# Performance work log

Measured on AMD Instinct MI355X. Metric: run time of the kernel, lower is better.

The kernel has to match this reference:

```python
import jax, jax.numpy as jnp
import numpy as np

N = 100000
E = 1600000
H = 128
IN = 16
OUT = 16
L = 3
G = 256  # number of graphs
EPS = 1e-12


def setup_inputs() -> dict:
    key = jax.random.key(0)
    ks = jax.random.split(key, 24)
    s = 0.05
    inp = {
        "x": jax.random.normal(ks[0], (N, IN), jnp.float32),
        "pos": jax.random.normal(ks[1], (N, 3), jnp.float32),
        "edge_index": jax.random.randint(ks[2], (2, E), 0, N, jnp.int64),
        "batch": jnp.sort(jax.random.randint(ks[3], (N,), 0, G, jnp.int64)),
        # node_lin: Linear(IN,H), ReLU, Linear(H,H)
        "node_W1": jax.random.normal(ks[4], (IN, H), jnp.float32) * s,
        "node_b1": jnp.zeros((H,), jnp.float32),
        "node_W2": jax.random.normal(ks[5], (H, H), jnp.float32) * s,
        "node_b2": jnp.zeros((H,), jnp.float32),
        # per-layer local_nn: Linear(H+4,H), ReLU, Linear(H,H)  (stacked over L)
        "local_W1": jax.random.normal(ks[6], (L, H + 4, H), jnp.float32) * s,
        "local_b1": jnp.zeros((L, H), jnp.float32),
        "local_W2": jax.random.normal(ks[7], (L, H, H), jnp.float32) * s,
        "local_b2": jnp.zeros((L, H), jnp.float32),
        # per-layer global_nn: Linear(H,H), ReLU, Linear(H,H)
        "global_W1": jax.random.normal(ks[8], (L, H, H), jnp.float32) * s,
        "global_b1": jnp.zeros((L, H), jnp.float32),
        "global_W2": jax.random.normal(ks[9], (L, H, H), jnp.float32) * s,
        "global_b2": jnp.zeros((L, H), jnp.float32),
        # heads
        "lin1_W": jax.random.normal(ks[10], (H, H // 2), jnp.float32) * s,
        "lin1_b": jnp.zeros((H // 2,), jnp.float32),
        "lin2_W": jax.random.normal(ks[11], (H // 2, OUT), jnp.float32) * s,
        "lin2_b": jnp.zeros((OUT,), jnp.float32),
    }
    return inp


def _angle(v1, v2):
    c = jnp.cross(v1, v2, axis=1)
    return jnp.arctan2(jnp.linalg.norm(c, axis=1), jnp.sum(v1 * v2, axis=1))


def reference(x, pos, edge_index, batch,
              node_W1, node_b1, node_W2, node_b2,
              local_W1, local_b1, local_W2, local_b2,
              global_W1, global_b1, global_W2, global_b2,
              lin1_W, lin1_b, lin2_W, lin2_b):
    src = edge_index[0]  # j (source)
    dst = edge_index[1]  # i (target, aggregation index)

    normal = pos / (jnp.linalg.norm(pos, axis=-1, keepdims=True) + EPS)

    pos_i, pos_j = pos[dst], pos[src]
    n_i, n_j = normal[dst], normal[src]
    pseudo = pos_j - pos_i  # [E, 3]
    # point-pair features [E, 4] (constant across layers since pos is fixed)
    ppf = jnp.stack([
        jnp.linalg.norm(pseudo, axis=1),
        _angle(n_i, pseudo),
        _angle(n_j, pseudo),
        _angle(n_i, n_j),
    ], axis=1)

    # node_lin (x is 2D -> MLP path; embedding path unused)
    h = jax.nn.relu(x @ node_W1 + node_b1) @ node_W2 + node_b2  # [N, H]

    for l in range(L):
        msg = jnp.concatenate([h[src], ppf], axis=1)  # [E, H+4]
        msg = jax.nn.relu(msg @ local_W1[l] + local_b1[l]) @ local_W2[l] + local_b2[l]
        agg = jax.ops.segment_sum(msg, dst, num_segments=N)  # scatter-add to nodes
        h = jax.nn.relu(agg @ global_W1[l] + global_b1[l]) @ global_W2[l] + global_b2[l]
        h = jax.nn.relu(h)

    out = jax.nn.relu(h @ lin1_W + lin1_b) @ lin2_W + lin2_b  # [N, OUT]
    return jax.ops.segment_sum(out, batch, num_segments=G)  # [G, OUT]
```

## Files before the change

kernel.cpp:

```cpp
#include <hip/hip_runtime.h>

#define NN 100000
#define NE 1600000
#define HD 128
#define NL 3
#define NG 256
#define NB 196
#define BCAP 56
#define BCAPTOT 10240

typedef __attribute__((ext_vector_type(8))) short short8;
typedef __attribute__((ext_vector_type(4))) float floatx4;
typedef __attribute__((ext_vector_type(2))) _Float16 half2v;

static __device__ __forceinline__ unsigned short f2bf(float f) {
    unsigned int u = __float_as_uint(f);
    u += 0x7fffu + ((u >> 16) & 1u);
    return (unsigned short)(u >> 16);
}
static __device__ __forceinline__ float bf2f(unsigned short h) {
    return __uint_as_float(((unsigned int)h) << 16);
}
static __device__ __forceinline__ float angle3(float ax, float ay, float az,
                                               float bx, float by, float bz) {
    float cx = ay*bz - az*by;
    float cy = az*bx - ax*bz;
    float cz = ax*by - ay*bx;
    float cn = sqrtf(cx*cx + cy*cy + cz*cz);
    float d  = ax*bx + ay*by + az*bz;
    return atan2f(cn, d);
}

union U32H2 { unsigned int u; half2v h; };
static __device__ __forceinline__ half2v u2h(unsigned int x) { U32H2 t; t.u = x; return t.h; }
static __device__ __forceinline__ unsigned int h2u(half2v x) { U32H2 t; t.h = x; return t.u; }


struct PrepSrcs { const float* p[14]; };

__global__ void k_prep(PrepSrcs s, unsigned short* __restrict__ dst) {
    int mat = blockIdx.y;
    int N = (mat == 13) ? 64 : 128;
    int e = blockIdx.x * 256 + threadIdx.x;
    if (e >= N * 128) return;
    int n = e >> 7, k = e & 127;
    dst[mat * 16384 + n * 128 + k] = f2bf(s.p[mat][k * N + n]);
}


__global__ void k_pn(const float* __restrict__ pos, float4* __restrict__ pn, int n) {
    int i = blockIdx.x * blockDim.x + threadIdx.x;
    if (i >= n) return;
    float x = pos[3*i], y = pos[3*i+1], z = pos[3*i+2];
    float inv = 1.0f / (sqrtf(x*x + y*y + z*z) + 1e-12f);
    pn[2*i]   = make_float4(x, y, z, 0.0f);
    pn[2*i+1] = make_float4(x*inv, y*inv, z*inv, 0.0f);
}


__global__ void k_binit(int* __restrict__ bcursor) {
    int b = threadIdx.x;
    if (b < NB) bcursor[b] = b * BCAPTOT;
}

__global__ __launch_bounds__(256) void k_bscatter(const int* __restrict__ ei,
                                                  int* __restrict__ bcursor,
                                                  unsigned int* __restrict__ bids, int e) {
    __shared__ int lcnt[NB];
    __shared__ unsigned int lbuf[NB * BCAP];
    int tid = threadIdx.x;
    for (int i = tid; i < NB; i += 256) lcnt[i] = 0;
    __syncthreads();
    int i0 = blockIdx.x * 4096 + tid * 16;
    if (i0 < e) {
#pragma unroll
        for (int q = 0; q < 4; q++) {
            int4 s4 = *(const int4*)(ei + i0 + q * 4);
            int4 d4 = *(const int4*)(ei + NE + i0 + q * 4);
            int ds[4] = {d4.x, d4.y, d4.z, d4.w};
            int ss[4] = {s4.x, s4.y, s4.z, s4.w};
#pragma unroll
            for (int r = 0; r < 4; r++) {
                int d = ds[r];
                int b = d >> 9;
                unsigned int w = ((unsigned int)(d & 511) << 17) | (unsigned int)ss[r];
                int pos = atomicAdd(&lcnt[b], 1);
                if (pos < BCAP) lbuf[b * BCAP + pos] = w;
                else { int p = atomicAdd(&bcursor[b], 1); bids[p] = w; }
            }
        }
    }
    __syncthreads();
    if (tid < NB) {
        int c = lcnt[tid];
        if (c > BCAP) c = BCAP;
        if (c > 0) {
            int base = atomicAdd(&bcursor[tid], c);
            for (int k = 0; k < c; k++) bids[base + k] = lbuf[tid * BCAP + k];
        }
    }
}

__global__ __launch_bounds__(256) void k_bfinal(const unsigned int* __restrict__ bids,
                                                const int* __restrict__ bcursor,
                                                int* __restrict__ ssrc,
                                                int* __restrict__ sdst,
                                                int* __restrict__ starts,
                                                int* __restrict__ deg) {
    __shared__ int s1[512];
    __shared__ int s2[256];
    int tid = threadIdx.x;
    int b = blockIdx.x;
    int node0 = b << 9;
    int base0 = b * BCAPTOT;
    int cnt = bcursor[b] - base0;
    s1[2 * tid] = 0; s1[2 * tid + 1] = 0;
    __syncthreads();
    for (int j = tid; j < cnt; j += 256)
        atomicAdd(&s1[bids[base0 + j] >> 17], 1);
    __syncthreads();
    int a0 = s1[2 * tid], a1 = s1[2 * tid + 1];
    s2[tid] = a0 + a1;
    __syncthreads();
    for (int off = 1; off < 256; off <<= 1) {
        int v = (tid >= off) ? s2[tid - off] : 0;
        __syncthreads();
        s2[tid] += v;
        __syncthreads();
    }
    int pairBase = (tid ? s2[tid - 1] : 0);
    int e0 = base0 + pairBase;
    int e1 = e0 + a0;
    int n0 = node0 + 2 * tid;
    if (n0 < NN)     { starts[n0] = e0;     deg[n0] = a0; }
    if (n0 + 1 < NN) { starts[n0 + 1] = e1; deg[n0 + 1] = a1; }
    s1[2 * tid] = e0; s1[2 * tid + 1] = e1;
    __syncthreads();
    for (int j = tid; j < cnt; j += 256) {
        unsigned int w = bids[base0 + j];
        int loc = w >> 17;
        int src = (int)(w & 0x1ffffu);
        int p = atomicAdd(&s1[loc], 1);
        ssrc[p] = src;
        sdst[p] = node0 + loc;
    }
}

__global__ void k_ppf_sorted(const int* __restrict__ ssrc, const int* __restrict__ sdst,
                             const float4* __restrict__ pn,
                             uint2* __restrict__ sppf, int npos) {
    int j = blockIdx.x * blockDim.x + threadIdx.x;
    if (j >= npos) return;
    unsigned int s = (unsigned int)ssrc[j];
    unsigned int d = (unsigned int)sdst[j];
    if (s >= NN || d >= NN) return;
    float4 ps_ = pn[2*s], ns_ = pn[2*s+1];
    float4 pd_ = pn[2*d], nd_ = pn[2*d+1];
    float px = ps_.x - pd_.x;
    float py = ps_.y - pd_.y;
    float pz = ps_.z - pd_.z;
    float f0 = sqrtf(px*px + py*py + pz*pz);
    float f1 = angle3(nd_.x, nd_.y, nd_.z, px, py, pz);
    float f2 = angle3(ns_.x, ns_.y, ns_.z, px, py, pz);
    float f3 = angle3(nd_.x, nd_.y, nd_.z, ns_.x, ns_.y, ns_.z);
    half2v h01 = { (_Float16)f0, (_Float16)f1 };
    half2v h23 = { (_Float16)f2, (_Float16)f3 };
    uint2 w;
    w.x = h2u(h01);
    w.y = h2u(h23);
    sppf[j] = w;
}


__global__ void k_node_lin1(const float* __restrict__ x, const float* __restrict__ W1,
                            const float* __restrict__ b1, unsigned short* __restrict__ u, int n) {
    __shared__ float sW[16 * HD];
    __shared__ float sb[HD];
    __shared__ float sx[16 * 16];
    int tid = threadIdx.x;
    for (int idx = tid; idx < 16 * HD; idx += 256) sW[idx] = W1[idx];
    if (tid < HD) sb[tid] = b1[tid];
    int r0 = blockIdx.x * 16;
    for (int idx = tid; idx < 16 * 16; idx += 256) {
        int r = r0 + (idx >> 4);
        sx[idx] = (r < n) ? x[r * 16 + (idx & 15)] : 0.0f;
    }
    __syncthreads();
    int col = tid & 127;
    int rsub = tid >> 7;
    float wcol[16];
#pragma unroll
    for (int k = 0; k < 16; k++) wcol[k] = sW[k * HD + col];
    float bb = sb[col];
    for (int rr = rsub; rr < 16; rr += 2) {
        int r = r0 + rr;
        if (r >= n) break;
        float acc = bb;
#pragma unroll
        for (int k = 0; k < 16; k++) acc = fmaf(sx[rr * 16 + k], wcol[k], acc);
        u[r * HD + col] = f2bf(fmaxf(acc, 0.0f));
    }
}


#define SKT 136

struct ChainArgs {
    const unsigned short* W[4];
    const float* bias[4];
    int epi[4];
};

template <int NS, int NCL>
__global__ __launch_bounds__(256, 4) void k_chain(
    const unsigned short* __restrict__ in, ChainArgs ca,
    const int* __restrict__ deg, unsigned short* __restrict__ out, int n) {
    __shared__ unsigned short LB[128 * SKT];
    __shared__ float sbias[NS][128];
    int tid = threadIdx.x;
    int wave = tid >> 6, lane = tid & 63, quad = lane >> 4, m = lane & 15;
    int rowBase = wave * 32;
    int gBase = blockIdx.x * 128;
    floatx4 z = {0.0f, 0.0f, 0.0f, 0.0f};
    short8 a[2][4];
#pragma unroll
    for (int rt = 0; rt < 2; rt++) {
        int r = gBase + rowBase + rt * 16 + m;
        int rc = r < n ? r : n - 1;
        const unsigned short* ap = in + (size_t)rc * 128 + quad * 8;
#pragma unroll
        for (int s = 0; s < 4; s++) a[rt][s] = *(const short8*)(ap + s * 32);
    }
    if (tid < 128) {
#pragma unroll
        for (int s = 0; s < NS; s++)
            if (ca.epi[s]) sbias[s][tid] = ca.bias[s][tid];
    }
    float dvd[2][4];
#pragma unroll
    for (int rt = 0; rt < 2; rt++)
#pragma unroll
        for (int r = 0; r < 4; r++) {
            int gr = gBase + rowBase + rt * 16 + quad * 4 + r;
            dvd[rt][r] = (float)deg[gr < n ? gr : n - 1];
        }

#pragma unroll
    for (int st = 0; st < NS; st++) {
        const int NC = (st == NS - 1) ? NCL : 128;
        if (st > 0) {
#pragma unroll
            for (int rt = 0; rt < 2; rt++) {
                const unsigned short* tp = &LB[(rowBase + rt * 16 + m) * SKT + quad * 8];
#pragma unroll
                for (int s = 0; s < 4; s++) a[rt][s] = *(const short8*)(tp + s * 32);
            }
            __syncthreads();
        }
        for (int idx = tid; idx < NC * 16; idx += 256) {
            int c = idx >> 4, k8 = idx & 15;
            *(short8*)&LB[c * SKT + k8 * 8] = ((const short8*)ca.W[st])[idx];
        }
        __syncthreads();

        floatx4 acc[2][8];
#pragma unroll
        for (int rt = 0; rt < 2; rt++)
#pragma unroll
            for (int ct = 0; ct < 8; ct++) acc[rt][ct] = z;
#pragma unroll
        for (int ct = 0; ct < NC / 16; ct++) {
            const unsigned short* bp = &LB[(ct * 16 + m) * SKT + quad * 8];
#pragma unroll
            for (int s = 0; s < 4; s++) {
                short8 b = *(const short8*)(bp + s * 32);
                acc[0][ct] = __builtin_amdgcn_mfma_f32_16x16x32_bf16(a[0][s], b, acc[0][ct], 0, 0, 0);
                acc[1][ct] = __builtin_amdgcn_mfma_f32_16x16x32_bf16(a[1][s], b, acc[1][ct], 0, 0, 0);
            }
        }
        __syncthreads();

        int epi = ca.epi[st];
#pragma unroll
        for (int ct = 0; ct < NC / 16; ct++) {
            int col = ct * 16 + m;
            float bv = epi ? sbias[st][col] : 0.0f;
#pragma unroll
            for (int rt = 0; rt < 2; rt++) {
#pragma unroll
                for (int r = 0; r < 4; r++) {
                    float v = acc[rt][ct][r];
                    if (epi == 1) v += bv;
                    else if (epi == 2) v += dvd[rt][r] * bv;
                    else if (epi == 3) v = fmaxf(v + bv, 0.0f);
                    unsigned short bw = f2bf(v);
                    int row = rowBase + rt * 16 + quad * 4 + r;
                    if (st == NS - 1) {
                        int gr = gBase + row;
                        if (gr < n) out[(size_t)gr * NCL + col] = bw;
                    } else {
                        LB[row * SKT + col] = bw;
                    }
                }
            }
        }
        if (st < NS - 1) __syncthreads();
    }
}


#if __has_builtin(__builtin_amdgcn_fdot2)
#define HAVE_FDOT2 1
#else
#define HAVE_FDOT2 0
#endif

static __device__ __forceinline__ void agg_edge(unsigned int u, uint2 q,
                                                half2v wA0, half2v wB0, half2v wA1, half2v wB1,
                                                float& a0, float& a1) {
    float tlo = __uint_as_float(u << 16);
    float thi = __uint_as_float(u & 0xffff0000u);
#if HAVE_FDOT2
    half2v p01 = u2h(q.x), p23 = u2h(q.y);
    float g0 = __builtin_amdgcn_fdot2(p01, wA0,
               __builtin_amdgcn_fdot2(p23, wB0, tlo, false), false);
    float g1 = __builtin_amdgcn_fdot2(p01, wA1,
               __builtin_amdgcn_fdot2(p23, wB1, thi, false), false);
#else
    half2v p01 = u2h(q.x), p23 = u2h(q.y);
    float px = (float)p01.x, py = (float)p01.y, pz = (float)p23.x, pw = (float)p23.y;
    float g0 = fmaf(px, (float)wA0.x, fmaf(py, (float)wA0.y,
               fmaf(pz, (float)wB0.x, fmaf(pw, (float)wB0.y, tlo))));
    float g1 = fmaf(px, (float)wA1.x, fmaf(py, (float)wA1.y,
               fmaf(pz, (float)wB1.x, fmaf(pw, (float)wB1.y, thi))));
#endif
    a0 += fmaxf(g0, 0.0f);
    a1 += fmaxf(g1, 0.0f);
}

#define GLOAD(u, off) \
    __asm__ volatile("global_load_dword %0, %1, %2" : "=v"(u) : "v"(off), "s"(t))

__global__ __launch_bounds__(256, 8) void k_agg(
    const int* __restrict__ starts, const int* __restrict__ deg,
    const int* __restrict__ ssrc,
    const uint2* __restrict__ sppf, const unsigned int* __restrict__ t,
    const float* __restrict__ W1p,
    unsigned int* __restrict__ S, int n) {
    int node = (blockIdx.x * 256 + threadIdx.x) >> 6;
    if (node >= n) return;
    int lane = threadIdx.x & 63;
    int c2 = lane * 2;
    float2 w0 = *(const float2*)(W1p + c2);
    float2 w1 = *(const float2*)(W1p + 128 + c2);
    float2 w2 = *(const float2*)(W1p + 256 + c2);
    float2 w3 = *(const float2*)(W1p + 384 + c2);
    half2v wA0 = { (_Float16)w0.x, (_Float16)w1.x };
    half2v wB0 = { (_Float16)w2.x, (_Float16)w3.x };
    half2v wA1 = { (_Float16)w0.y, (_Float16)w1.y };
    half2v wB1 = { (_Float16)w2.y, (_Float16)w3.y };
    int e0 = __builtin_amdgcn_readfirstlane(starts[node]);
    int dg = __builtin_amdgcn_readfirstlane(deg[node]);
    int e1 = e0 + dg;
    unsigned int lane4 = (unsigned int)lane * 4u;
    float a0 = 0.0f, a1 = 0.0f;
    int e = e0;
    for (; e + 8 <= e1; e += 8) {
        int s0 = ssrc[e],     s1 = ssrc[e + 1], s2 = ssrc[e + 2], s3 = ssrc[e + 3];
        int s4 = ssrc[e + 4], s5 = ssrc[e + 5], s6 = ssrc[e + 6], s7 = ssrc[e + 7];
        uint2 q0 = sppf[e],     q1 = sppf[e + 1], q2 = sppf[e + 2], q3 = sppf[e + 3];
        uint2 q4 = sppf[e + 4], q5 = sppf[e + 5], q6 = sppf[e + 6], q7 = sppf[e + 7];
        unsigned int u0, u1, u2, u3, u4, u5, u6, u7;
        GLOAD(u0, ((unsigned)s0 << 8) | lane4);
        GLOAD(u1, ((unsigned)s1 << 8) | lane4);
        GLOAD(u2, ((unsigned)s2 << 8) | lane4);
        GLOAD(u3, ((unsigned)s3 << 8) | lane4);
        GLOAD(u4, ((unsigned)s4 << 8) | lane4);
        GLOAD(u5, ((unsigned)s5 << 8) | lane4);
        GLOAD(u6, ((unsigned)s6 << 8) | lane4);
        GLOAD(u7, ((unsigned)s7 << 8) | lane4);
        __asm__ volatile("s_waitcnt vmcnt(0)"
                         : "+v"(u0), "+v"(u1), "+v"(u2), "+v"(u3),
                           "+v"(u4), "+v"(u5), "+v"(u6), "+v"(u7));
        agg_edge(u0, q0, wA0, wB0, wA1, wB1, a0, a1);
        agg_edge(u1, q1, wA0, wB0, wA1, wB1, a0, a1);
        agg_edge(u2, q2, wA0, wB0, wA1, wB1, a0, a1);
        agg_edge(u3, q3, wA0, wB0, wA1, wB1, a0, a1);
        agg_edge(u4, q4, wA0, wB0, wA1, wB1, a0, a1);
        agg_edge(u5, q5, wA0, wB0, wA1, wB1, a0, a1);
        agg_edge(u6, q6, wA0, wB0, wA1, wB1, a0, a1);
        agg_edge(u7, q7, wA0, wB0, wA1, wB1, a0, a1);
    }
    if (e + 4 <= e1) {
        int s0 = ssrc[e], s1 = ssrc[e + 1], s2 = ssrc[e + 2], s3 = ssrc[e + 3];
        uint2 q0 = sppf[e], q1 = sppf[e + 1], q2 = sppf[e + 2], q3 = sppf[e + 3];
        unsigned int u0, u1, u2, u3;
        GLOAD(u0, ((unsigned)s0 << 8) | lane4);
        GLOAD(u1, ((unsigned)s1 << 8) | lane4);
        GLOAD(u2, ((unsigned)s2 << 8) | lane4);
        GLOAD(u3, ((unsigned)s3 << 8) | lane4);
        __asm__ volatile("s_waitcnt vmcnt(0)"
                         : "+v"(u0), "+v"(u1), "+v"(u2), "+v"(u3));
        agg_edge(u0, q0, wA0, wB0, wA1, wB1, a0, a1);
        agg_edge(u1, q1, wA0, wB0, wA1, wB1, a0, a1);
        agg_edge(u2, q2, wA0, wB0, wA1, wB1, a0, a1);
        agg_edge(u3, q3, wA0, wB0, wA1, wB1, a0, a1);
        e += 4;
    }
    for (; e < e1; e++) {
        int s0 = ssrc[e];
        uint2 q0 = sppf[e];
        unsigned int u0 = t[((unsigned)s0 << 6) | lane];
        agg_edge(u0, q0, wA0, wB0, wA1, wB1, a0, a1);
    }
    unsigned int r = ((unsigned int)f2bf(a1) << 16) | f2bf(a0);
    S[(size_t)node * 64 + lane] = r;
}


__global__ void k_head2(const unsigned short* __restrict__ v, const float* __restrict__ W,
                        const float* __restrict__ b, const int* __restrict__ batch,
                        float* __restrict__ outg, int n) {
    __shared__ float sW[64 * 16];
    __shared__ float sb[16];
    __shared__ float sacc[64][17];
    __shared__ int sbid[64];
    int tid = threadIdx.x;
    for (int idx = tid; idx < 64 * 16; idx += 256) sW[idx] = W[idx];
    if (tid < 16) sb[tid] = b[tid];
    int r0 = blockIdx.x * 64;
    if (tid < 64) {
        int r = r0 + tid;
        sbid[tid] = (r < n) ? batch[r] : -1;
    }
    __syncthreads();
    int rl = tid >> 4, c = tid & 15;
#pragma unroll
    for (int i = 0; i < 4; i++) {
        int row = rl + i * 16;
        int r = r0 + row;
        float acc = 0.0f;
        if (r < n) {
            const unsigned int* vr = (const unsigned int*)(v + (size_t)r * 64);
            acc = sb[c];
#pragma unroll
            for (int k2 = 0; k2 < 32; k2++) {
                unsigned int u = vr[k2];
                acc = fmaf(__uint_as_float(u << 16), sW[(2 * k2) * 16 + c], acc);
                acc = fmaf(__uint_as_float(u & 0xffff0000u), sW[(2 * k2 + 1) * 16 + c], acc);
            }
        }
        sacc[row][c] = acc;
    }
    __syncthreads();
    if (tid < 16) {
        int cc = tid;
        float run = 0.0f;
        int cur = sbid[0];
        for (int row = 0; row < 64; row++) {
            int bid = sbid[row];
            if (bid != cur) {
                if (cur >= 0) atomicAdd(&outg[cur * 16 + cc], run);
                run = 0.0f;
                cur = bid;
            }
            run += sacc[row][cc];
        }
        if (cur >= 0) atomicAdd(&outg[cur * 16 + cc], run);
    }
}


extern "C" void kernel_launch(void* const* d_in, const int* in_sizes, int n_in,
                              void* d_out, int out_size, void* d_ws, size_t ws_size,
                              hipStream_t stream) {
    (void)in_sizes; (void)n_in; (void)out_size; (void)ws_size;
    const float* x    = (const float*)d_in[0];
    const float* pos  = (const float*)d_in[1];
    const int*   ei   = (const int*)d_in[2];
    const int*   batch= (const int*)d_in[3];
    const float* nW1  = (const float*)d_in[4];
    const float* nb1  = (const float*)d_in[5];
    const float* nW2  = (const float*)d_in[6];
    const float* nb2  = (const float*)d_in[7];
    const float* lW1  = (const float*)d_in[8];
    const float* lb1  = (const float*)d_in[9];
    const float* lW2  = (const float*)d_in[10];
    const float* lb2  = (const float*)d_in[11];
    const float* gW1  = (const float*)d_in[12];
    const float* gb1  = (const float*)d_in[13];
    const float* gW2  = (const float*)d_in[14];
    const float* gb2  = (const float*)d_in[15];
    const float* l1W  = (const float*)d_in[16];
    const float* l1b  = (const float*)d_in[17];
    const float* l2W  = (const float*)d_in[18];
    const float* l2b  = (const float*)d_in[19];
    float* outg = (float*)d_out;

    const int NPOS = NB * BCAPTOT;

    char* ws = (char*)d_ws;
    size_t off = 0;
    auto alloc = [&](size_t bytes) -> void* {
        void* p = ws + off;
        off = (off + bytes + 255) & ~(size_t)255;
        return p;
    };
    unsigned short* P0 = (unsigned short*)alloc((size_t)NN * HD * 2);
    unsigned short* P1 = (unsigned short*)alloc((size_t)NN * HD * 2);
    uint2* sppf  = (uint2*)alloc((size_t)NPOS * 8);
    int* ssrc    = (int*)alloc((size_t)NPOS * 4);
    float4* pn   = (float4*)alloc((size_t)NN * 32);
    int* deg     = (int*)alloc((size_t)NN * 4);
    int* starts  = (int*)alloc((size_t)(NN + 2) * 4);
    int* bcursor = (int*)alloc((size_t)(NB + 2) * 4);
    unsigned short* pw = (unsigned short*)alloc((size_t)14 * 16384 * 2);
    unsigned int* bids = (unsigned int*)P0;
    int* sdst          = (int*)P1;

    PrepSrcs ps;
    ps.p[0] = nW2;
    for (int l = 0; l < 3; l++) {
        ps.p[1 + l] = lW1 + (size_t)l * 132 * 128;
        ps.p[4 + l] = lW2 + (size_t)l * 16384;
        ps.p[7 + l] = gW1 + (size_t)l * 16384;
        ps.p[10 + l] = gW2 + (size_t)l * 16384;
    }
    ps.p[13] = l1W;

    hipMemsetAsync(outg, 0, (size_t)NG * 16 * 4, stream);

    k_prep<<<dim3(64, 14), 256, 0, stream>>>(ps, pw);
    k_pn<<<(NN + 255) / 256, 256, 0, stream>>>(pos, pn, NN);
    k_binit<<<1, 256, 0, stream>>>(bcursor);
    const int NTILE = (NE + 4095) / 4096;
    k_bscatter<<<NTILE, 256, 0, stream>>>(ei, bcursor, bids, NE);
    k_bfinal<<<NB, 256, 0, stream>>>(bids, bcursor, ssrc, sdst, starts, deg);
    k_ppf_sorted<<<(NPOS + 255) / 256, 256, 0, stream>>>(ssrc, sdst, pn, sppf, NPOS);

    k_node_lin1<<<(NN + 15) / 16, 256, 0, stream>>>(x, nW1, nb1, P1, NN);

    const int GB = (NN + 127) / 128;
    const int AGB = (NN * 64 + 255) / 256;

    {
        ChainArgs ca;
        ca.W[0] = pw;                      ca.bias[0] = nb2;  ca.epi[0] = 1;
        ca.W[1] = pw + (size_t)1 * 16384;  ca.bias[1] = lb1;  ca.epi[1] = 1;
        ca.W[2] = nullptr; ca.bias[2] = nullptr; ca.epi[2] = 0;
        ca.W[3] = nullptr; ca.bias[3] = nullptr; ca.epi[3] = 0;
        k_chain<2, 128><<<GB, 256, 0, stream>>>(P1, ca, deg, P0, NN);
    }

    unsigned short* tbuf = P0;
    unsigned short* sbuf = P1;
    for (int l = 0; l < NL; l++) {
        const float* W1p = lW1 + (size_t)l * 132 * 128 + 128 * 128;
        k_agg<<<AGB, 256, 0, stream>>>(starts, deg, ssrc, sppf,
                                       (const unsigned int*)tbuf, W1p,
                                       (unsigned int*)sbuf, NN);
        ChainArgs ca;
        ca.W[0] = pw + (size_t)(4 + l) * 16384;  ca.bias[0] = lb2 + l * 128; ca.epi[0] = 2;
        ca.W[1] = pw + (size_t)(7 + l) * 16384;  ca.bias[1] = gb1 + l * 128; ca.epi[1] = 3;
        ca.W[2] = pw + (size_t)(10 + l) * 16384; ca.bias[2] = gb2 + l * 128; ca.epi[2] = 3;
        if (l < NL - 1) {
            ca.W[3] = pw + (size_t)(2 + l) * 16384;
            ca.bias[3] = lb1 + (l + 1) * 128;
            ca.epi[3] = 1;
            k_chain<4, 128><<<GB, 256, 0, stream>>>(sbuf, ca, deg, tbuf, NN);
        } else {
            ca.W[3] = pw + (size_t)13 * 16384;
            ca.bias[3] = l1b; ca.epi[3] = 3;
            k_chain<4, 64><<<GB, 256, 0, stream>>>(sbuf, ca, deg, tbuf, NN);
        }
    }
    k_head2<<<(NN + 63) / 64, 256, 0, stream>>>(tbuf, l2W, l2b, batch, outg, NN);
}
```

Baseline: 509.6 us.

## Fuse PPF computation into bucket finalize and transpose MFMA operands for packed stores

```diff
diff --git a/kernel.cpp b/kernel.cpp
--- a/kernel.cpp
+++ b/kernel.cpp
@@ -103,8 +103,9 @@
 
 __global__ __launch_bounds__(256) void k_bfinal(const unsigned int* __restrict__ bids,
                                                 const int* __restrict__ bcursor,
+                                                const float4* __restrict__ pn,
                                                 int* __restrict__ ssrc,
-                                                int* __restrict__ sdst,
+                                                uint2* __restrict__ sppf,
                                                 int* __restrict__ starts,
                                                 int* __restrict__ deg) {
     __shared__ int s1[512];
@@ -141,34 +142,24 @@
         int loc = w >> 17;
         int src = (int)(w & 0x1ffffu);
         int p = atomicAdd(&s1[loc], 1);
+        int dst = node0 + loc;
         ssrc[p] = src;
-        sdst[p] = node0 + loc;
-    }
-}
-
-__global__ void k_ppf_sorted(const int* __restrict__ ssrc, const int* __restrict__ sdst,
-                             const float4* __restrict__ pn,
-                             uint2* __restrict__ sppf, int npos) {
-    int j = blockIdx.x * blockDim.x + threadIdx.x;
-    if (j >= npos) return;
-    unsigned int s = (unsigned int)ssrc[j];
-    unsigned int d = (unsigned int)sdst[j];
-    if (s >= NN || d >= NN) return;
-    float4 ps_ = pn[2*s], ns_ = pn[2*s+1];
-    float4 pd_ = pn[2*d], nd_ = pn[2*d+1];
-    float px = ps_.x - pd_.x;
-    float py = ps_.y - pd_.y;
-    float pz = ps_.z - pd_.z;
-    float f0 = sqrtf(px*px + py*py + pz*pz);
-    float f1 = angle3(nd_.x, nd_.y, nd_.z, px, py, pz);
-    float f2 = angle3(ns_.x, ns_.y, ns_.z, px, py, pz);
-    float f3 = angle3(nd_.x, nd_.y, nd_.z, ns_.x, ns_.y, ns_.z);
-    half2v h01 = { (_Float16)f0, (_Float16)f1 };
-    half2v h23 = { (_Float16)f2, (_Float16)f3 };
-    uint2 w;
-    w.x = h2u(h01);
-    w.y = h2u(h23);
-    sppf[j] = w;
+        float4 ps_ = pn[2*src], ns_ = pn[2*src+1];
+        float4 pd_ = pn[2*dst], nd_ = pn[2*dst+1];
+        float px = ps_.x - pd_.x;
+        float py = ps_.y - pd_.y;
+        float pz = ps_.z - pd_.z;
+        float f0 = sqrtf(px*px + py*py + pz*pz);
+        float f1 = angle3(nd_.x, nd_.y, nd_.z, px, py, pz);
+        float f2 = angle3(ns_.x, ns_.y, ns_.z, px, py, pz);
+        float f3 = angle3(nd_.x, nd_.y, nd_.z, ns_.x, ns_.y, ns_.z);
+        half2v h01 = { (_Float16)f0, (_Float16)f1 };
+        half2v h23 = { (_Float16)f2, (_Float16)f3 };
+        uint2 wv;
+        wv.x = h2u(h01);
+        wv.y = h2u(h23);
+        sppf[p] = wv;
+    }
 }
 
 
@@ -222,38 +213,36 @@
     int rowBase = wave * 32;
     int gBase = blockIdx.x * 128;
     floatx4 z = {0.0f, 0.0f, 0.0f, 0.0f};
-    short8 a[2][4];
-#pragma unroll
-    for (int rt = 0; rt < 2; rt++) {
-        int r = gBase + rowBase + rt * 16 + m;
+    short8 x[2][4];
+#pragma unroll
+    for (int jt = 0; jt < 2; jt++) {
+        int r = gBase + rowBase + jt * 16 + m;
         int rc = r < n ? r : n - 1;
         const unsigned short* ap = in + (size_t)rc * 128 + quad * 8;
 #pragma unroll
-        for (int s = 0; s < 4; s++) a[rt][s] = *(const short8*)(ap + s * 32);
+        for (int s = 0; s < 4; s++) x[jt][s] = *(const short8*)(ap + s * 32);
     }
     if (tid < 128) {
 #pragma unroll
         for (int s = 0; s < NS; s++)
             if (ca.epi[s]) sbias[s][tid] = ca.bias[s][tid];
     }
-    float dvd[2][4];
-#pragma unroll
-    for (int rt = 0; rt < 2; rt++)
-#pragma unroll
-        for (int r = 0; r < 4; r++) {
-            int gr = gBase + rowBase + rt * 16 + quad * 4 + r;
-            dvd[rt][r] = (float)deg[gr < n ? gr : n - 1];
-        }
+    float dvd[2];
+#pragma unroll
+    for (int jt = 0; jt < 2; jt++) {
+        int gr = gBase + rowBase + jt * 16 + m;
+        dvd[jt] = (float)deg[gr < n ? gr : n - 1];
+    }
 
 #pragma unroll
     for (int st = 0; st < NS; st++) {
         const int NC = (st == NS - 1) ? NCL : 128;
         if (st > 0) {
 #pragma unroll
-            for (int rt = 0; rt < 2; rt++) {
-                const unsigned short* tp = &LB[(rowBase + rt * 16 + m) * SKT + quad * 8];
-#pragma unroll
-                for (int s = 0; s < 4; s++) a[rt][s] = *(const short8*)(tp + s * 32);
+            for (int jt = 0; jt < 2; jt++) {
+                const unsigned short* tp = &LB[(rowBase + jt * 16 + m) * SKT + quad * 8];
+#pragma unroll
+                for (int s = 0; s < 4; s++) x[jt][s] = *(const short8*)(tp + s * 32);
             }
             __syncthreads();
         }
@@ -265,42 +254,45 @@
 
         floatx4 acc[2][8];
 #pragma unroll
-        for (int rt = 0; rt < 2; rt++)
-#pragma unroll
-            for (int ct = 0; ct < 8; ct++) acc[rt][ct] = z;
+        for (int jt = 0; jt < 2; jt++)
+#pragma unroll
+            for (int ct = 0; ct < 8; ct++) acc[jt][ct] = z;
 #pragma unroll
         for (int ct = 0; ct < NC / 16; ct++) {
-            const unsigned short* bp = &LB[(ct * 16 + m) * SKT + quad * 8];
+            const unsigned short* wp = &LB[(ct * 16 + m) * SKT + quad * 8];
 #pragma unroll
             for (int s = 0; s < 4; s++) {
-                short8 b = *(const short8*)(bp + s * 32);
-                acc[0][ct] = __builtin_amdgcn_mfma_f32_16x16x32_bf16(a[0][s], b, acc[0][ct], 0, 0, 0);
-                acc[1][ct] = __builtin_amdgcn_mfma_f32_16x16x32_bf16(a[1][s], b, acc[1][ct], 0, 0, 0);
+                short8 w = *(const short8*)(wp + s * 32);
+                acc[0][ct] = __builtin_amdgcn_mfma_f32_16x16x32_bf16(w, x[0][s], acc[0][ct], 0, 0, 0);
+                acc[1][ct] = __builtin_amdgcn_mfma_f32_16x16x32_bf16(w, x[1][s], acc[1][ct], 0, 0, 0);
             }
         }
         __syncthreads();
 
         int epi = ca.epi[st];
 #pragma unroll
-        for (int ct = 0; ct < NC / 16; ct++) {
-            int col = ct * 16 + m;
-            float bv = epi ? sbias[st][col] : 0.0f;
-#pragma unroll
-            for (int rt = 0; rt < 2; rt++) {
+        for (int jt = 0; jt < 2; jt++) {
+            int row = rowBase + jt * 16 + m;
+            int gr = gBase + row;
+#pragma unroll
+            for (int ct = 0; ct < NC / 16; ct++) {
+                int c0 = ct * 16 + quad * 4;
+                float4 bb4 = epi ? *(const float4*)&sbias[st][c0]
+                                 : make_float4(0.f, 0.f, 0.f, 0.f);
+                float bvs[4] = {bb4.x, bb4.y, bb4.z, bb4.w};
+                unsigned short pk[4];
 #pragma unroll
                 for (int r = 0; r < 4; r++) {
-                    float v = acc[rt][ct][r];
-                    if (epi == 1) v += bv;
-                    else if (epi == 2) v += dvd[rt][r] * bv;
-                    else if (epi == 3) v = fmaxf(v + bv, 0.0f);
-                    unsigned short bw = f2bf(v);
-                    int row = rowBase + rt * 16 + quad * 4 + r;
-                    if (st == NS - 1) {
-                        int gr = gBase + row;
-                        if (gr < n) out[(size_t)gr * NCL + col] = bw;
-                    } else {
-                        LB[row * SKT + col] = bw;
-                    }
+                    float v = acc[jt][ct][r];
+                    if (epi == 1) v += bvs[r];
+                    else if (epi == 2) v += dvd[jt] * bvs[r];
+                    else if (epi == 3) v = fmaxf(v + bvs[r], 0.0f);
+                    pk[r] = f2bf(v);
+                }
+                if (st == NS - 1) {
+                    if (gr < n) *(uint2*)&out[(size_t)gr * NCL + c0] = *(uint2*)pk;
+                } else {
+                    *(uint2*)&LB[row * SKT + c0] = *(uint2*)pk;
                 }
             }
         }
@@ -516,7 +508,6 @@
     int* bcursor = (int*)alloc((size_t)(NB + 2) * 4);
     unsigned short* pw = (unsigned short*)alloc((size_t)14 * 16384 * 2);
     unsigned int* bids = (unsigned int*)P0;
-    int* sdst          = (int*)P1;
 
     PrepSrcs ps;
     ps.p[0] = nW2;
@@ -535,8 +526,7 @@
     k_binit<<<1, 256, 0, stream>>>(bcursor);
     const int NTILE = (NE + 4095) / 4096;
     k_bscatter<<<NTILE, 256, 0, stream>>>(ei, bcursor, bids, NE);
-    k_bfinal<<<NB, 256, 0, stream>>>(bids, bcursor, ssrc, sdst, starts, deg);
-    k_ppf_sorted<<<(NPOS + 255) / 256, 256, 0, stream>>>(ssrc, sdst, pn, sppf, NPOS);
+    k_bfinal<<<NB, 256, 0, stream>>>(bids, bcursor, pn, ssrc, sppf, starts, deg);
 
     k_node_lin1<<<(NN + 15) / 16, 256, 0, stream>>>(x, nW1, nb1, P1, NN);
 
```

Result: slower. 531.3 us (+4.3%).
